# Performance work log

Hardware: AMD Instinct MI355X
Metric: run time of the kernel (lower is better)

Reference implementation:

```python
import jax, jax.numpy as jnp
import numpy as np

EPS = 1e-8

def cos_sim(a, b, axis=-1):
    # torch.nn.functional.cosine_similarity: dot / max(|a|*|b|, eps)
    num = jnp.sum(a * b, axis=axis)
    den = jnp.maximum(jnp.linalg.norm(a, axis=axis) * jnp.linalg.norm(b, axis=axis), EPS)
    return num / den

def address_similarity(address, addresses):
    # address: [b, d], addresses: [b, n, d] -> [b, n]
    return cos_sim(address[:, None, :], addresses, axis=2)

def kv_insert(state_k, state_v, k, x, eps=EPS):
    # state_k/state_v: [b, n, d]; k: [b, d]; x: [b, d] (or [1, d], broadcast)
    alpha = cos_sim(k[:, None, :], state_k, axis=2)          # [b, n]
    alpha = jnp.where(alpha > eps, alpha, 0.0)
    return (1.0 - alpha)[..., None] * state_v + alpha[..., None] * x[:, None, :]

def replace(new_value, prev_value, tensr):
    # new_value/prev_value: [b, d]; tensr: [b, n, d]
    sim_to = cos_sim(prev_value[:, None, :], tensr, axis=2)  # [b, n]
    return tensr * (1.0 - sim_to)[..., None] + sim_to[..., None] * new_value[:, None, :]

def select_address(address, addresses, list_of_values):
    cs = address_similarity(address, addresses)              # [b, n]
    return [jnp.sum(values * cs[..., None], axis=1) for values in list_of_values]

def setup_inputs() -> dict:
    key = jax.random.key(0)
    ks = jax.random.split(key, 5)
    B, N, D = 32, 2048, 128
    return {
        "at_addr": jax.random.normal(ks[0], (B, D), dtype=jnp.float32),
        "addresses": jax.random.normal(ks[1], (B, N, D), dtype=jnp.float32),
        "tags": jax.random.normal(ks[2], (B, N, D), dtype=jnp.float32),
        "col1": jax.random.normal(ks[3], (B, N, D), dtype=jnp.float32),
        "col2": jax.random.normal(ks[4], (B, N, D), dtype=jnp.float32),
        "zero_vec": jnp.zeros((D,), dtype=jnp.float32),
        "gc_steps": 2,
    }

def reference(at_addr, addresses, tags, col1, col2, zero_vec, gc_steps):
    B = at_addr.shape[0]
    zv = jnp.broadcast_to(zero_vec[None, :], (B, zero_vec.shape[0]))
    # dereference the App node
    fn_addr, arg_addr = select_address(at_addr, addresses, [col1, col2])
    fn_tag, param_addr, body_addr = select_address(fn_addr, addresses, [tags, col1, col2])
    a_tag, a_l, a_r = select_address(arg_addr, addresses, [tags, col1, col2])
    # substitute arg into param's slot (globally scoped vars)
    tags = kv_insert(addresses, tags, param_addr, a_tag)
    col1 = kv_insert(addresses, col1, param_addr, a_l)
    col2 = kv_insert(addresses, col2, param_addr, a_r)
    col1 = replace(arg_addr, param_addr, col1)
    col2 = replace(arg_addr, param_addr, col2)
    # write the fn body over the App node
    b_tag, b_l, b_r = select_address(body_addr, addresses, [tags, col1, col2])
    tags = kv_insert(addresses, tags, at_addr, b_tag)
    col1 = kv_insert(addresses, col1, at_addr, b_l)
    col2 = kv_insert(addresses, col2, at_addr, b_r)
    # garbage collection
    for _ in range(gc_steps):
        for gaddr in (fn_addr, param_addr, body_addr):
            tags = kv_insert(addresses, tags, gaddr, zv)
            col1 = kv_insert(addresses, col1, gaddr, zv)
            col2 = kv_insert(addresses, col2, gaddr, zv)
    return (tags, col1, col2)
```

## Files before the change

### kernel.cpp

```cpp
#include <hip/hip_runtime.h>

#define EPSF 1e-8f
#define DD 128

__device__ __forceinline__ float4 ld4(const float* p){ return *reinterpret_cast<const float4*>(p); }
__device__ __forceinline__ void st4(float* p, const float4& v){ *reinterpret_cast<float4*>(p) = v; }
__device__ __forceinline__ float dot4(const float4& a, const float4& b){
  return a.x*b.x + a.y*b.y + a.z*b.z + a.w*b.w;
}
__device__ __forceinline__ void fma4(float4& acc, const float4& a, float s){
  acc.x += a.x*s; acc.y += a.y*s; acc.z += a.z*s; acc.w += a.w*s;
}
__device__ __forceinline__ float4 mix4(float a, const float4& v, const float4& x){
  float4 r;
  r.x = (1.f-a)*v.x + a*x.x;
  r.y = (1.f-a)*v.y + a*x.y;
  r.z = (1.f-a)*v.z + a*x.z;
  r.w = (1.f-a)*v.w + a*x.w;
  return r;
}
__device__ __forceinline__ float red32(float v){
  v += __shfl_xor(v, 1);
  v += __shfl_xor(v, 2);
  v += __shfl_xor(v, 4);
  v += __shfl_xor(v, 8);
  v += __shfl_xor(v, 16);
  return v;
}
__device__ __forceinline__ void block_red(float* red, int group, int l, int t,
                                          const float4& acc, float* dst){
  red[group*DD + l*4+0] = acc.x;
  red[group*DD + l*4+1] = acc.y;
  red[group*DD + l*4+2] = acc.z;
  red[group*DD + l*4+3] = acc.w;
  __syncthreads();
  if (t < DD){
    float s = 0.f;
    #pragma unroll
    for (int g = 0; g < 8; ++g) s += red[g*DD + t];
    dst[t] = s;
  }
  __syncthreads();
}

__global__ __launch_bounds__(256) void kA(const float* __restrict__ at,
                                          const float* __restrict__ addr,
                                          const float* __restrict__ col1,
                                          const float* __restrict__ col2,
                                          float* __restrict__ cs0,
                                          float* __restrict__ naf,
                                          float* __restrict__ part,
                                          int B, int N, int chunks){
  __shared__ float red[8*DD];
  int blk = blockIdx.x;
  int b = blk / chunks, c = blk % chunks;
  int rows = N / chunks, n0 = c * rows;
  int t = threadIdx.x, lane = t & 63, wave = t >> 6, l = lane & 31;
  int group = wave*2 + (lane >> 5);

  float4 at4 = ld4(at + (size_t)b*DD + l*4);
  float nat = sqrtf(red32(dot4(at4, at4)));

  float4 accF = make_float4(0,0,0,0), accA = make_float4(0,0,0,0);
  for (int r = group; r < rows; r += 8){
    size_t n = (size_t)n0 + r;
    size_t off = ((size_t)b*N + n)*DD + l*4;
    float4 a4 = ld4(addr + off);
    float4 c1 = ld4(col1 + off), c2 = ld4(col2 + off);
    float dp = red32(dot4(at4, a4));
    float n2 = red32(dot4(a4, a4));
    float na = sqrtf(n2);
    float cs = dp / fmaxf(nat * na, EPSF);
    if (l == 0){ cs0[(size_t)b*N + n] = cs; naf[(size_t)b*N + n] = na; }
    fma4(accF, c1, cs);
    fma4(accA, c2, cs);
  }
  block_red(red, group, l, t, accF, part + (((size_t)(0*B + b))*chunks + c)*DD);
  block_red(red, group, l, t, accA, part + (((size_t)(1*B + b))*chunks + c)*DD);
}

__global__ void kFin(const float* __restrict__ part, float* __restrict__ dst,
                     int nvec, int B, int chunks){
  int i = blockIdx.x*blockDim.x + threadIdx.x;
  int total = nvec * B * DD;
  if (i >= total) return;
  int d = i & (DD-1);
  int vb = i >> 7;
  const float* p = part + ((size_t)vb*chunks)*DD + d;
  float s = 0.f;
  for (int c = 0; c < chunks; ++c) s += p[(size_t)c*DD];
  dst[i] = s;
}

__global__ __launch_bounds__(256) void kB(const float* __restrict__ addr,
                                          const float* __restrict__ tags,
                                          const float* __restrict__ col1,
                                          const float* __restrict__ col2,
                                          const float* __restrict__ vecs,
                                          const float* __restrict__ naf,
                                          float* __restrict__ csfn,
                                          float* __restrict__ part,
                                          int B, int N, int chunks){
  __shared__ float red[8*DD];
  int blk = blockIdx.x;
  int b = blk / chunks, c = blk % chunks;
  int rows = N / chunks, n0 = c * rows;
  int t = threadIdx.x, lane = t & 63, wave = t >> 6, l = lane & 31;
  int group = wave*2 + (lane >> 5);

  float4 fn4 = ld4(vecs + ((size_t)0*B + b)*DD + l*4);
  float4 ag4 = ld4(vecs + ((size_t)1*B + b)*DD + l*4);
  float nfn = sqrtf(red32(dot4(fn4, fn4)));
  float nag = sqrtf(red32(dot4(ag4, ag4)));

  float4 accP = make_float4(0,0,0,0), accB = accP, accT = accP, accL = accP, accR = accP;
  for (int r = group; r < rows; r += 8){
    size_t n = (size_t)n0 + r;
    size_t off = ((size_t)b*N + n)*DD + l*4;
    float4 a4 = ld4(addr + off);
    float4 t4 = ld4(tags + off), c1 = ld4(col1 + off), c2 = ld4(col2 + off);
    float na = naf[(size_t)b*N + n];
    float dfn = red32(dot4(fn4, a4));
    float dag = red32(dot4(ag4, a4));
    float cf = dfn / fmaxf(nfn*na, EPSF);
    float ca = dag / fmaxf(nag*na, EPSF);
    if (l == 0) csfn[(size_t)b*N + n] = cf;
    fma4(accP, c1, cf);
    fma4(accB, c2, cf);
    fma4(accT, t4, ca);
    fma4(accL, c1, ca);
    fma4(accR, c2, ca);
  }
  block_red(red, group, l, t, accP, part + (((size_t)(0*B + b))*chunks + c)*DD);
  block_red(red, group, l, t, accB, part + (((size_t)(1*B + b))*chunks + c)*DD);
  block_red(red, group, l, t, accT, part + (((size_t)(2*B + b))*chunks + c)*DD);
  block_red(red, group, l, t, accL, part + (((size_t)(3*B + b))*chunks + c)*DD);
  block_red(red, group, l, t, accR, part + (((size_t)(4*B + b))*chunks + c)*DD);
}

__global__ __launch_bounds__(256) void kC(const float* __restrict__ addr,
                                          const float* __restrict__ tags,
                                          const float* __restrict__ col1,
                                          const float* __restrict__ col2,
                                          const float* __restrict__ vecs,
                                          const float* __restrict__ naf,
                                          float* __restrict__ alphap,
                                          float* __restrict__ csbody,
                                          float* __restrict__ s1f,
                                          float* __restrict__ s2f,
                                          float* __restrict__ part,
                                          int B, int N, int chunks){
  __shared__ float red[8*DD];
  int blk = blockIdx.x;
  int b = blk / chunks, c = blk % chunks;
  int rows = N / chunks, n0 = c * rows;
  int t = threadIdx.x, lane = t & 63, wave = t >> 6, l = lane & 31;
  int group = wave*2 + (lane >> 5);

  size_t BD = (size_t)B*DD;
  float4 ag4 = ld4(vecs + 1*BD + (size_t)b*DD + l*4);
  float4 pm4 = ld4(vecs + 2*BD + (size_t)b*DD + l*4);
  float4 bd4 = ld4(vecs + 3*BD + (size_t)b*DD + l*4);
  float4 xt4 = ld4(vecs + 4*BD + (size_t)b*DD + l*4);
  float4 xl4 = ld4(vecs + 5*BD + (size_t)b*DD + l*4);
  float4 xr4 = ld4(vecs + 6*BD + (size_t)b*DD + l*4);
  float npm = sqrtf(red32(dot4(pm4, pm4)));
  float nbd = sqrtf(red32(dot4(bd4, bd4)));

  float4 accT = make_float4(0,0,0,0), accL = accT, accR = accT;
  for (int r = group; r < rows; r += 8){
    size_t n = (size_t)n0 + r;
    size_t off = ((size_t)b*N + n)*DD + l*4;
    float4 a4 = ld4(addr + off);
    float4 t4 = ld4(tags + off), c1 = ld4(col1 + off), c2 = ld4(col2 + off);
    float na = naf[(size_t)b*N + n];
    float dp  = red32(dot4(pm4, a4));
    float db  = red32(dot4(bd4, a4));
    float csp = dp / fmaxf(npm*na, EPSF);
    float ap  = csp > EPSF ? csp : 0.f;
    float csb = db / fmaxf(nbd*na, EPSF);

    float4 tn  = mix4(ap, t4, xt4);
    float4 c1n = mix4(ap, c1, xl4);
    float4 c2n = mix4(ap, c2, xr4);
    float d1  = red32(dot4(pm4, c1n));
    float n21 = red32(dot4(c1n, c1n));
    float s1 = d1 / fmaxf(npm * sqrtf(n21), EPSF);
    float4 c1f = mix4(s1, c1n, ag4);
    float d2  = red32(dot4(pm4, c2n));
    float n22 = red32(dot4(c2n, c2n));
    float s2 = d2 / fmaxf(npm * sqrtf(n22), EPSF);
    float4 c2f = mix4(s2, c2n, ag4);

    if (l == 0){
      alphap[(size_t)b*N + n] = ap;
      csbody[(size_t)b*N + n] = csb;
      s1f[(size_t)b*N + n] = s1;
      s2f[(size_t)b*N + n] = s2;
    }
    fma4(accT, tn,  csb);
    fma4(accL, c1f, csb);
    fma4(accR, c2f, csb);
  }
  block_red(red, group, l, t, accT, part + (((size_t)(0*B + b))*chunks + c)*DD);
  block_red(red, group, l, t, accL, part + (((size_t)(1*B + b))*chunks + c)*DD);
  block_red(red, group, l, t, accR, part + (((size_t)(2*B + b))*chunks + c)*DD);
}

__global__ __launch_bounds__(256) void kE(const float* __restrict__ tags,
                                          const float* __restrict__ col1,
                                          const float* __restrict__ col2,
                                          float* __restrict__ o_t,
                                          float* __restrict__ o_1,
                                          float* __restrict__ o_2,
                                          const float* __restrict__ cs0,
                                          const float* __restrict__ csfn,
                                          const float* __restrict__ alphap,
                                          const float* __restrict__ csbody,
                                          const float* __restrict__ s1f,
                                          const float* __restrict__ s2f,
                                          const float* __restrict__ vecs,
                                          const float* __restrict__ zv,
                                          const int* __restrict__ gcp,
                                          int B, int N){
  size_t i = (size_t)blockIdx.x*blockDim.x + threadIdx.x;
  size_t total = (size_t)B*N*(DD/4);
  if (i >= total) return;
  int l = (int)(i & 31);
  size_t bn = i >> 5;
  int b = (int)(bn / (size_t)N);

  float ap = alphap[bn], s1 = s1f[bn], s2 = s2f[bn];
  float c0 = cs0[bn], cf = csfn[bn], cb = csbody[bn];
  float aat = c0 > EPSF ? c0 : 0.f;
  float af  = cf > EPSF ? cf : 0.f;
  float ab  = cb > EPSF ? cb : 0.f;
  float q = (1.f-af)*(1.f-ap)*(1.f-ab);
  int gc = gcp[0];
  float P = 1.f;
  for (int k = 0; k < gc; ++k) P *= q;

  size_t BD = (size_t)B*DD;
  const float* vb = vecs + (size_t)b*DD + (size_t)l*4;
  float4 ag = ld4(vb + 1*BD);
  float4 xt = ld4(vb + 4*BD), xl = ld4(vb + 5*BD), xr = ld4(vb + 6*BD);
  float4 bt = ld4(vb + 7*BD), bl = ld4(vb + 8*BD), br = ld4(vb + 9*BD);
  float4 z4 = ld4(zv + l*4);

  size_t off = bn*DD + (size_t)l*4;
  float4 t4 = ld4(tags + off), c1 = ld4(col1 + off), c2 = ld4(col2 + off);

  float4 tn  = mix4(ap, t4, xt);
  float4 c1f = mix4(s1, mix4(ap, c1, xl), ag);
  float4 c2f = mix4(s2, mix4(ap, c2, xr), ag);

  float4 u;
  u = mix4(aat, tn, bt);
  u.x = P*u.x + (1.f-P)*z4.x; u.y = P*u.y + (1.f-P)*z4.y;
  u.z = P*u.z + (1.f-P)*z4.z; u.w = P*u.w + (1.f-P)*z4.w;
  st4(o_t + off, u);
  u = mix4(aat, c1f, bl);
  u.x = P*u.x + (1.f-P)*z4.x; u.y = P*u.y + (1.f-P)*z4.y;
  u.z = P*u.z + (1.f-P)*z4.z; u.w = P*u.w + (1.f-P)*z4.w;
  st4(o_1 + off, u);
  u = mix4(aat, c2f, br);
  u.x = P*u.x + (1.f-P)*z4.x; u.y = P*u.y + (1.f-P)*z4.y;
  u.z = P*u.z + (1.f-P)*z4.z; u.w = P*u.w + (1.f-P)*z4.w;
  st4(o_2 + off, u);
}

extern "C" void kernel_launch(void* const* d_in, const int* in_sizes, int n_in,
                              void* d_out, int out_size, void* d_ws, size_t ws_size,
                              hipStream_t stream){
  const float* at   = (const float*)d_in[0];
  const float* addr = (const float*)d_in[1];
  const float* tags = (const float*)d_in[2];
  const float* col1 = (const float*)d_in[3];
  const float* col2 = (const float*)d_in[4];
  const float* zv   = (const float*)d_in[5];
  const int*   gc   = (const int*)d_in[6];

  int Dd = in_sizes[5];
  int B  = in_sizes[0] / Dd;
  int N  = in_sizes[1] / in_sizes[0];
  (void)Dd;

  size_t S  = (size_t)B * N;
  size_t BD = (size_t)B * DD;

  int CH = 64;
  while (CH > 1){
    size_t need = (7*S + 10*BD + (size_t)5*B*CH*DD) * sizeof(float);
    if (need <= ws_size && (N % CH) == 0) break;
    CH >>= 1;
  }

  float* w = (float*)d_ws;
  float* cs0    = w;
  float* csfn   = w + S;
  float* alphap = w + 2*S;
  float* csbody = w + 3*S;
  float* s1f    = w + 4*S;
  float* s2f    = w + 5*S;
  float* naf    = w + 6*S;
  float* vecs   = w + 7*S;
  float* part   = vecs + 10*BD;

  float* o_t = (float*)d_out;
  float* o_1 = o_t + (size_t)B*N*DD;
  float* o_2 = o_1 + (size_t)B*N*DD;

  dim3 blk(256);
  dim3 grid(B*CH);

  kA<<<grid, blk, 0, stream>>>(at, addr, col1, col2, cs0, naf, part, B, N, CH);
  {
    int tot = 2*B*DD;
    kFin<<<(tot+255)/256, 256, 0, stream>>>(part, vecs + 0*BD, 2, B, CH);
  }
  kB<<<grid, blk, 0, stream>>>(addr, tags, col1, col2, vecs, naf, csfn, part, B, N, CH);
  {
    int tot = 5*B*DD;
    kFin<<<(tot+255)/256, 256, 0, stream>>>(part, vecs + 2*BD, 5, B, CH);
  }
  kC<<<grid, blk, 0, stream>>>(addr, tags, col1, col2, vecs, naf, alphap, csbody,
                               s1f, s2f, part, B, N, CH);
  {
    int tot = 3*B*DD;
    kFin<<<(tot+255)/256, 256, 0, stream>>>(part, vecs + 7*BD, 3, B, CH);
  }
  {
    size_t tot = (size_t)B*N*(DD/4);
    kE<<<(unsigned)((tot+255)/256), 256, 0, stream>>>(tags, col1, col2, o_t, o_1, o_2,
                                                      cs0, csfn, alphap, csbody,
                                                      s1f, s2f, vecs, zv, gc, B, N);
  }
}
```

Baseline: 152.8 us.

## Use 16-lane row groups with two float4 halves per thread in kA/kB/kC

Each row of 128 floats is now handled by 16 lanes holding two float4 halves each, rather than 32 lanes holding one. This cuts one shuffle stage from every cross-lane reduction and doubles the number of rows a block processes at once (16 groups). The loops are unrolled by two, and the chunk count is halved from 64 to 32. The shared reduction buffer doubles in size and register pressure rises, which may reduce occupancy.

```diff
diff --git a/kernel.cpp b/kernel.cpp
--- a/kernel.cpp
+++ b/kernel.cpp
@@ -19,25 +19,29 @@
   r.w = (1.f-a)*v.w + a*x.w;
   return r;
 }
-__device__ __forceinline__ float red32(float v){
+__device__ __forceinline__ float red16(float v){
   v += __shfl_xor(v, 1);
   v += __shfl_xor(v, 2);
   v += __shfl_xor(v, 4);
   v += __shfl_xor(v, 8);
-  v += __shfl_xor(v, 16);
   return v;
 }
-__device__ __forceinline__ void block_red(float* red, int group, int l, int t,
-                                          const float4& acc, float* dst){
-  red[group*DD + l*4+0] = acc.x;
-  red[group*DD + l*4+1] = acc.y;
-  red[group*DD + l*4+2] = acc.z;
-  red[group*DD + l*4+3] = acc.w;
+__device__ __forceinline__ void block_red16(float* red, int g, int l, int t,
+                                            const float4& accA, const float4& accB,
+                                            float* dst){
+  red[g*DD + l*4+0] = accA.x;
+  red[g*DD + l*4+1] = accA.y;
+  red[g*DD + l*4+2] = accA.z;
+  red[g*DD + l*4+3] = accA.w;
+  red[g*DD + 64 + l*4+0] = accB.x;
+  red[g*DD + 64 + l*4+1] = accB.y;
+  red[g*DD + 64 + l*4+2] = accB.z;
+  red[g*DD + 64 + l*4+3] = accB.w;
   __syncthreads();
   if (t < DD){
     float s = 0.f;
     #pragma unroll
-    for (int g = 0; g < 8; ++g) s += red[g*DD + t];
+    for (int q = 0; q < 16; ++q) s += red[q*DD + t];
     dst[t] = s;
   }
   __syncthreads();
@@ -51,32 +55,35 @@
                                           float* __restrict__ naf,
                                           float* __restrict__ part,
                                           int B, int N, int chunks){
-  __shared__ float red[8*DD];
+  __shared__ float red[16*DD];
   int blk = blockIdx.x;
   int b = blk / chunks, c = blk % chunks;
   int rows = N / chunks, n0 = c * rows;
-  int t = threadIdx.x, lane = t & 63, wave = t >> 6, l = lane & 31;
-  int group = wave*2 + (lane >> 5);
-
-  float4 at4 = ld4(at + (size_t)b*DD + l*4);
-  float nat = sqrtf(red32(dot4(at4, at4)));
-
-  float4 accF = make_float4(0,0,0,0), accA = make_float4(0,0,0,0);
-  for (int r = group; r < rows; r += 8){
+  int t = threadIdx.x, g = t >> 4, l = t & 15;
+  size_t bN = (size_t)b * N;
+
+  const float* atp = at + (size_t)b*DD;
+  float4 atA = ld4(atp + l*4), atB = ld4(atp + 64 + l*4);
+  float nat = sqrtf(red16(dot4(atA, atA) + dot4(atB, atB)));
+
+  float4 accFA = make_float4(0,0,0,0), accFB = accFA, accAA = accFA, accAB = accFA;
+  #pragma unroll 2
+  for (int r = g; r < rows; r += 16){
     size_t n = (size_t)n0 + r;
-    size_t off = ((size_t)b*N + n)*DD + l*4;
-    float4 a4 = ld4(addr + off);
-    float4 c1 = ld4(col1 + off), c2 = ld4(col2 + off);
-    float dp = red32(dot4(at4, a4));
-    float n2 = red32(dot4(a4, a4));
+    size_t base = (bN + n)*DD;
+    float4 aA  = ld4(addr + base + l*4), aB  = ld4(addr + base + 64 + l*4);
+    float4 c1A = ld4(col1 + base + l*4), c1B = ld4(col1 + base + 64 + l*4);
+    float4 c2A = ld4(col2 + base + l*4), c2B = ld4(col2 + base + 64 + l*4);
+    float dp = red16(dot4(atA, aA) + dot4(atB, aB));
+    float n2 = red16(dot4(aA, aA) + dot4(aB, aB));
     float na = sqrtf(n2);
     float cs = dp / fmaxf(nat * na, EPSF);
-    if (l == 0){ cs0[(size_t)b*N + n] = cs; naf[(size_t)b*N + n] = na; }
-    fma4(accF, c1, cs);
-    fma4(accA, c2, cs);
-  }
-  block_red(red, group, l, t, accF, part + (((size_t)(0*B + b))*chunks + c)*DD);
-  block_red(red, group, l, t, accA, part + (((size_t)(1*B + b))*chunks + c)*DD);
+    if (l == 0){ cs0[bN + n] = cs; naf[bN + n] = na; }
+    fma4(accFA, c1A, cs); fma4(accFB, c1B, cs);
+    fma4(accAA, c2A, cs); fma4(accAB, c2B, cs);
+  }
+  block_red16(red, g, l, t, accFA, accFB, part + (((size_t)(0*B + b))*chunks + c)*DD);
+  block_red16(red, g, l, t, accAA, accAB, part + (((size_t)(1*B + b))*chunks + c)*DD);
 }
 
 __global__ void kFin(const float* __restrict__ part, float* __restrict__ dst,
@@ -101,41 +108,47 @@
                                           float* __restrict__ csfn,
                                           float* __restrict__ part,
                                           int B, int N, int chunks){
-  __shared__ float red[8*DD];
+  __shared__ float red[16*DD];
   int blk = blockIdx.x;
   int b = blk / chunks, c = blk % chunks;
   int rows = N / chunks, n0 = c * rows;
-  int t = threadIdx.x, lane = t & 63, wave = t >> 6, l = lane & 31;
-  int group = wave*2 + (lane >> 5);
-
-  float4 fn4 = ld4(vecs + ((size_t)0*B + b)*DD + l*4);
-  float4 ag4 = ld4(vecs + ((size_t)1*B + b)*DD + l*4);
-  float nfn = sqrtf(red32(dot4(fn4, fn4)));
-  float nag = sqrtf(red32(dot4(ag4, ag4)));
-
-  float4 accP = make_float4(0,0,0,0), accB = accP, accT = accP, accL = accP, accR = accP;
-  for (int r = group; r < rows; r += 8){
+  int t = threadIdx.x, g = t >> 4, l = t & 15;
+  size_t bN = (size_t)b * N;
+
+  const float* fnp = vecs + ((size_t)0*B + b)*DD;
+  const float* agp = vecs + ((size_t)1*B + b)*DD;
+  float4 fnA = ld4(fnp + l*4), fnB = ld4(fnp + 64 + l*4);
+  float4 agA = ld4(agp + l*4), agB = ld4(agp + 64 + l*4);
+  float nfn = sqrtf(red16(dot4(fnA, fnA) + dot4(fnB, fnB)));
+  float nag = sqrtf(red16(dot4(agA, agA) + dot4(agB, agB)));
+
+  float4 z = make_float4(0,0,0,0);
+  float4 accPA=z, accPB=z, accBA=z, accBB=z, accTA=z, accTB=z, accLA=z, accLB=z, accRA=z, accRB=z;
+  #pragma unroll 2
+  for (int r = g; r < rows; r += 16){
     size_t n = (size_t)n0 + r;
-    size_t off = ((size_t)b*N + n)*DD + l*4;
-    float4 a4 = ld4(addr + off);
-    float4 t4 = ld4(tags + off), c1 = ld4(col1 + off), c2 = ld4(col2 + off);
-    float na = naf[(size_t)b*N + n];
-    float dfn = red32(dot4(fn4, a4));
-    float dag = red32(dot4(ag4, a4));
+    size_t base = (bN + n)*DD;
+    float4 aA  = ld4(addr + base + l*4), aB  = ld4(addr + base + 64 + l*4);
+    float4 t4A = ld4(tags + base + l*4), t4B = ld4(tags + base + 64 + l*4);
+    float4 c1A = ld4(col1 + base + l*4), c1B = ld4(col1 + base + 64 + l*4);
+    float4 c2A = ld4(col2 + base + l*4), c2B = ld4(col2 + base + 64 + l*4);
+    float na = naf[bN + n];
+    float dfn = red16(dot4(fnA, aA) + dot4(fnB, aB));
+    float dag = red16(dot4(agA, aA) + dot4(agB, aB));
     float cf = dfn / fmaxf(nfn*na, EPSF);
     float ca = dag / fmaxf(nag*na, EPSF);
-    if (l == 0) csfn[(size_t)b*N + n] = cf;
-    fma4(accP, c1, cf);
-    fma4(accB, c2, cf);
-    fma4(accT, t4, ca);
-    fma4(accL, c1, ca);
-    fma4(accR, c2, ca);
-  }
-  block_red(red, group, l, t, accP, part + (((size_t)(0*B + b))*chunks + c)*DD);
-  block_red(red, group, l, t, accB, part + (((size_t)(1*B + b))*chunks + c)*DD);
-  block_red(red, group, l, t, accT, part + (((size_t)(2*B + b))*chunks + c)*DD);
-  block_red(red, group, l, t, accL, part + (((size_t)(3*B + b))*chunks + c)*DD);
-  block_red(red, group, l, t, accR, part + (((size_t)(4*B + b))*chunks + c)*DD);
+    if (l == 0) csfn[bN + n] = cf;
+    fma4(accPA, c1A, cf); fma4(accPB, c1B, cf);
+    fma4(accBA, c2A, cf); fma4(accBB, c2B, cf);
+    fma4(accTA, t4A, ca); fma4(accTB, t4B, ca);
+    fma4(accLA, c1A, ca); fma4(accLB, c1B, ca);
+    fma4(accRA, c2A, ca); fma4(accRB, c2B, ca);
+  }
+  block_red16(red, g, l, t, accPA, accPB, part + (((size_t)(0*B + b))*chunks + c)*DD);
+  block_red16(red, g, l, t, accBA, accBB, part + (((size_t)(1*B + b))*chunks + c)*DD);
+  block_red16(red, g, l, t, accTA, accTB, part + (((size_t)(2*B + b))*chunks + c)*DD);
+  block_red16(red, g, l, t, accLA, accLB, part + (((size_t)(3*B + b))*chunks + c)*DD);
+  block_red16(red, g, l, t, accRA, accRB, part + (((size_t)(4*B + b))*chunks + c)*DD);
 }
 
 __global__ __launch_bounds__(256) void kC(const float* __restrict__ addr,
@@ -150,61 +163,66 @@
                                           float* __restrict__ s2f,
                                           float* __restrict__ part,
                                           int B, int N, int chunks){
-  __shared__ float red[8*DD];
+  __shared__ float red[16*DD];
   int blk = blockIdx.x;
   int b = blk / chunks, c = blk % chunks;
   int rows = N / chunks, n0 = c * rows;
-  int t = threadIdx.x, lane = t & 63, wave = t >> 6, l = lane & 31;
-  int group = wave*2 + (lane >> 5);
+  int t = threadIdx.x, g = t >> 4, l = t & 15;
+  size_t bN = (size_t)b * N;
 
   size_t BD = (size_t)B*DD;
-  float4 ag4 = ld4(vecs + 1*BD + (size_t)b*DD + l*4);
-  float4 pm4 = ld4(vecs + 2*BD + (size_t)b*DD + l*4);
-  float4 bd4 = ld4(vecs + 3*BD + (size_t)b*DD + l*4);
-  float4 xt4 = ld4(vecs + 4*BD + (size_t)b*DD + l*4);
-  float4 xl4 = ld4(vecs + 5*BD + (size_t)b*DD + l*4);
-  float4 xr4 = ld4(vecs + 6*BD + (size_t)b*DD + l*4);
-  float npm = sqrtf(red32(dot4(pm4, pm4)));
-  float nbd = sqrtf(red32(dot4(bd4, bd4)));
-
-  float4 accT = make_float4(0,0,0,0), accL = accT, accR = accT;
-  for (int r = group; r < rows; r += 8){
+  const float* vp = vecs + (size_t)b*DD;
+  float4 agA = ld4(vp + 1*BD + l*4), agB = ld4(vp + 1*BD + 64 + l*4);
+  float4 pmA = ld4(vp + 2*BD + l*4), pmB = ld4(vp + 2*BD + 64 + l*4);
+  float4 bdA = ld4(vp + 3*BD + l*4), bdB = ld4(vp + 3*BD + 64 + l*4);
+  float4 xtA = ld4(vp + 4*BD + l*4), xtB = ld4(vp + 4*BD + 64 + l*4);
+  float4 xlA = ld4(vp + 5*BD + l*4), xlB = ld4(vp + 5*BD + 64 + l*4);
+  float4 xrA = ld4(vp + 6*BD + l*4), xrB = ld4(vp + 6*BD + 64 + l*4);
+  float npm = sqrtf(red16(dot4(pmA, pmA) + dot4(pmB, pmB)));
+  float nbd = sqrtf(red16(dot4(bdA, bdA) + dot4(bdB, bdB)));
+
+  float4 z = make_float4(0,0,0,0);
+  float4 accTA=z, accTB=z, accLA=z, accLB=z, accRA=z, accRB=z;
+  #pragma unroll 2
+  for (int r = g; r < rows; r += 16){
     size_t n = (size_t)n0 + r;
-    size_t off = ((size_t)b*N + n)*DD + l*4;
-    float4 a4 = ld4(addr + off);
-    float4 t4 = ld4(tags + off), c1 = ld4(col1 + off), c2 = ld4(col2 + off);
-    float na = naf[(size_t)b*N + n];
-    float dp  = red32(dot4(pm4, a4));
-    float db  = red32(dot4(bd4, a4));
+    size_t base = (bN + n)*DD;
+    float4 aA  = ld4(addr + base + l*4), aB  = ld4(addr + base + 64 + l*4);
+    float4 t4A = ld4(tags + base + l*4), t4B = ld4(tags + base + 64 + l*4);
+    float4 c1A = ld4(col1 + base + l*4), c1B = ld4(col1 + base + 64 + l*4);
+    float4 c2A = ld4(col2 + base + l*4), c2B = ld4(col2 + base + 64 + l*4);
+    float na = naf[bN + n];
+    float dp = red16(dot4(pmA, aA) + dot4(pmB, aB));
+    float db = red16(dot4(bdA, aA) + dot4(bdB, aB));
     float csp = dp / fmaxf(npm*na, EPSF);
     float ap  = csp > EPSF ? csp : 0.f;
     float csb = db / fmaxf(nbd*na, EPSF);
 
-    float4 tn  = mix4(ap, t4, xt4);
-    float4 c1n = mix4(ap, c1, xl4);
-    float4 c2n = mix4(ap, c2, xr4);
-    float d1  = red32(dot4(pm4, c1n));
-    float n21 = red32(dot4(c1n, c1n));
+    float4 tnA  = mix4(ap, t4A, xtA), tnB  = mix4(ap, t4B, xtB);
+    float4 c1nA = mix4(ap, c1A, xlA), c1nB = mix4(ap, c1B, xlB);
+    float4 c2nA = mix4(ap, c2A, xrA), c2nB = mix4(ap, c2B, xrB);
+    float d1  = red16(dot4(pmA, c1nA) + dot4(pmB, c1nB));
+    float n21 = red16(dot4(c1nA, c1nA) + dot4(c1nB, c1nB));
     float s1 = d1 / fmaxf(npm * sqrtf(n21), EPSF);
-    float4 c1f = mix4(s1, c1n, ag4);
-    float d2  = red32(dot4(pm4, c2n));
-    float n22 = red32(dot4(c2n, c2n));
+    float4 c1fA = mix4(s1, c1nA, agA), c1fB = mix4(s1, c1nB, agB);
+    float d2  = red16(dot4(pmA, c2nA) + dot4(pmB, c2nB));
+    float n22 = red16(dot4(c2nA, c2nA) + dot4(c2nB, c2nB));
     float s2 = d2 / fmaxf(npm * sqrtf(n22), EPSF);
-    float4 c2f = mix4(s2, c2n, ag4);
+    float4 c2fA = mix4(s2, c2nA, agA), c2fB = mix4(s2, c2nB, agB);
 
     if (l == 0){
-      alphap[(size_t)b*N + n] = ap;
-      csbody[(size_t)b*N + n] = csb;
-      s1f[(size_t)b*N + n] = s1;
-      s2f[(size_t)b*N + n] = s2;
+      alphap[bN + n] = ap;
+      csbody[bN + n] = csb;
+      s1f[bN + n] = s1;
+      s2f[bN + n] = s2;
     }
-    fma4(accT, tn,  csb);
-    fma4(accL, c1f, csb);
-    fma4(accR, c2f, csb);
-  }
-  block_red(red, group, l, t, accT, part + (((size_t)(0*B + b))*chunks + c)*DD);
-  block_red(red, group, l, t, accL, part + (((size_t)(1*B + b))*chunks + c)*DD);
-  block_red(red, group, l, t, accR, part + (((size_t)(2*B + b))*chunks + c)*DD);
+    fma4(accTA, tnA,  csb); fma4(accTB, tnB,  csb);
+    fma4(accLA, c1fA, csb); fma4(accLB, c1fB, csb);
+    fma4(accRA, c2fA, csb); fma4(accRB, c2fB, csb);
+  }
+  block_red16(red, g, l, t, accTA, accTB, part + (((size_t)(0*B + b))*chunks + c)*DD);
+  block_red16(red, g, l, t, accLA, accLB, part + (((size_t)(1*B + b))*chunks + c)*DD);
+  block_red16(red, g, l, t, accRA, accRB, part + (((size_t)(2*B + b))*chunks + c)*DD);
 }
 
 __global__ __launch_bounds__(256) void kE(const float* __restrict__ tags,
@@ -288,7 +306,7 @@
   size_t S  = (size_t)B * N;
   size_t BD = (size_t)B * DD;
 
-  int CH = 64;
+  int CH = 32;
   while (CH > 1){
     size_t need = (7*S + 10*BD + (size_t)5*B*CH*DD) * sizeof(float);
     if (need <= ws_size && (N % CH) == 0) break;
```

Measured after the change: 126.3 us. -17.4%, faster.
